# Optimization experiments

Measured on AMD Instinct MI355X. Metric: run time of the kernel, lower is better.

The kernel has to match this reference:

```python
import jax, jax.numpy as jnp
import numpy as np

N_EXPERTS = 64
TOP_K = 8
NORM_TOPK = True
SCALING = 1.0


def setup_inputs() -> dict:
    key = jax.random.key(0)
    logits = jax.random.normal(key, (524288, N_EXPERTS), dtype=jnp.float32)
    return {"logits": logits}


def reference(logits):
    # scoring_func == 'softmax': softmax over expert dim in float32
    routing_weights = jax.nn.softmax(logits.astype(jnp.float32), axis=1)
    # top-k experts per token: values and indices, sorted descending (matches torch.topk)
    topk_weights, topk_ids = jax.lax.top_k(routing_weights, TOP_K)  # [T, K]
    if NORM_TOPK:
        topk_weights = topk_weights / jnp.sum(topk_weights, axis=-1, keepdims=True)
    if SCALING != 1.0:
        topk_weights = topk_weights * SCALING
    # torch.histc(topk_ids, bins=E, min=0, max=E) == bincount over flat ids (float output)
    tokens_per_expert = jnp.zeros((N_EXPERTS,), dtype=jnp.float32).at[topk_ids.ravel()].add(1.0)
    return (logits, routing_weights, topk_weights, topk_ids, tokens_per_expert)
```

## Files before the change

kernel.cpp:

```cpp
#include <hip/hip_runtime.h>
#include <math.h>

#define NEXP 64
#define TOPK 8
#define TTILE 256
#define PITCH 65
#define NPROD 4
#define BLKT 512
#define GRID 256

typedef float v4 __attribute__((ext_vector_type(4)));

#define FAST_BAR() do {                                       \
    __builtin_amdgcn_sched_barrier(0);                        \
    asm volatile("s_waitcnt lgkmcnt(0)" ::: "memory");        \
    __builtin_amdgcn_s_barrier();                             \
    __builtin_amdgcn_sched_barrier(0);                        \
} while (0)

__global__ __launch_bounds__(BLKT) void router_kernel(
    const float* __restrict__ logits,
    float* __restrict__ out_logits,
    float* __restrict__ out_rw,
    float* __restrict__ out_tw,
    float* __restrict__ out_ti,
    float* __restrict__ out_hist,
    int nT)
{
    __shared__ float lds[2][TTILE * PITCH];
    __shared__ float srow[2][TTILE];
    __shared__ float shist[NEXP];

    const int tid  = threadIdx.x;
    const int wid  = tid >> 6;
    const int l    = tid & 63;
    const bool prod = wid < NPROD;
    if (tid < NEXP) shist[tid] = 0.0f;

    const int G = gridDim.x;
    int tb = blockIdx.x;
    v4 regs[16];

    if (prod && tb < nT) {
        const long base = (long)tb * (TTILE * NEXP / 4);
        const v4* g = (const v4*)logits + base;
        #pragma unroll
        for (int k = 0; k < 16; ++k)
            regs[k] = __builtin_nontemporal_load(&g[(wid << 6) + l + (k << 8)]);
        v4* gp = (v4*)out_logits + base;
        #pragma unroll
        for (int k = 0; k < 16; ++k) {
            int i = (wid << 6) + l + (k << 8);
            v4 v = regs[k];
            gp[i] = v;
            int r = i >> 4, c4 = (i & 15) << 2;
            float* b = &lds[0][r * PITCH + c4];
            b[0] = v.x; b[1] = v.y; b[2] = v.z; b[3] = v.w;
        }
    }
    FAST_BAR();

    int it = 0;
    for (; tb < nT; ++it, tb += G) {
        const int cur = it & 1;
        const int nxt = cur ^ 1;
        const int tb_next = tb + G;

        if (prod) {
            if (tb_next < nT) {
                const v4* g = (const v4*)logits + (long)tb_next * (TTILE * NEXP / 4);
                #pragma unroll
                for (int k = 0; k < 16; ++k)
                    regs[k] = __builtin_nontemporal_load(&g[(wid << 6) + l + (k << 8)]);
            }
            if (it > 0) {
                v4* grw = (v4*)out_rw + (long)(tb - G) * (TTILE * NEXP / 4);
                #pragma unroll
                for (int k = 0; k < 16; ++k) {
                    int i = (wid << 6) + l + (k << 8);
                    int r = i >> 4, c4 = (i & 15) << 2;
                    float si = srow[nxt][r];
                    const float* b = &lds[nxt][r * PITCH + c4];
                    v4 o = { b[0] * si, b[1] * si, b[2] * si, b[3] * si };
                    grw[i] = o;
                }
            }
            if (tb_next < nT) {
                v4* gp = (v4*)out_logits + (long)tb_next * (TTILE * NEXP / 4);
                #pragma unroll
                for (int k = 0; k < 16; ++k) {
                    int i = (wid << 6) + l + (k << 8);
                    v4 v = regs[k];
                    gp[i] = v;
                    int r = i >> 4, c4 = (i & 15) << 2;
                    float* b = &lds[nxt][r * PITCH + c4];
                    b[0] = v.x; b[1] = v.y; b[2] = v.z; b[3] = v.w;
                }
            }
        } else {
            const int t = ((wid - NPROD) << 6) + l;
            float* __restrict__ row = &lds[cur][t * PITCH];
            float vals[TOPK], ids[TOPK];
            #pragma unroll
            for (int j = 0; j < TOPK; ++j) { vals[j] = -INFINITY; ids[j] = 0.0f; }
            float ssum = 0.0f;

            #pragma unroll 8
            for (int e = 0; e < NEXP; ++e) {
                float x  = row[e];
                float ev = __expf(x);
                ssum += ev;
                row[e] = ev;
                float fe = (float)e;
                bool c[TOPK];
                #pragma unroll
                for (int j = 0; j < TOPK; ++j) c[j] = x > vals[j];
                #pragma unroll
                for (int j = TOPK - 1; j >= 1; --j) {
                    ids[j]  = c[j] ? (c[j - 1] ? ids[j - 1] : fe) : ids[j];
                    vals[j] = __builtin_amdgcn_fmed3f(x, vals[j - 1], vals[j]);
                }
                ids[0]  = c[0] ? fe : ids[0];
                vals[0] = fmaxf(vals[0], x);
            }
            const float sinv = 1.0f / ssum;
            srow[cur][t] = sinv;

            float ew[TOPK];
            float tsum = 0.0f;
            #pragma unroll
            for (int j = 0; j < TOPK; ++j) { ew[j] = __expf(vals[j]); tsum += ew[j]; }
            const float tinv = 1.0f / tsum;

            const long tok = (long)tb * TTILE + t;
            v4* twp = (v4*)out_tw + tok * 2;
            v4* tip = (v4*)out_ti + tok * 2;
            v4 w0 = { ew[0] * tinv, ew[1] * tinv, ew[2] * tinv, ew[3] * tinv };
            v4 w1 = { ew[4] * tinv, ew[5] * tinv, ew[6] * tinv, ew[7] * tinv };
            v4 i0 = { ids[0], ids[1], ids[2], ids[3] };
            v4 i1 = { ids[4], ids[5], ids[6], ids[7] };
            twp[0] = w0; twp[1] = w1;
            tip[0] = i0; tip[1] = i1;

            #pragma unroll
            for (int j = 0; j < TOPK; ++j)
                atomicAdd(&shist[(int)ids[j]], 1.0f);
        }
        FAST_BAR();
    }

    if (prod && it > 0) {
        const int lastpar = (it - 1) & 1;
        v4* grw = (v4*)out_rw + (long)(tb - G) * (TTILE * NEXP / 4);
        #pragma unroll
        for (int k = 0; k < 16; ++k) {
            int i = (wid << 6) + l + (k << 8);
            int r = i >> 4, c4 = (i & 15) << 2;
            float si = srow[lastpar][r];
            const float* b = &lds[lastpar][r * PITCH + c4];
            v4 o = { b[0] * si, b[1] * si, b[2] * si, b[3] * si };
            grw[i] = o;
        }
    }
    __syncthreads();
    if (tid < NEXP) atomicAdd(&out_hist[tid], shist[tid]);
}

extern "C" void kernel_launch(void* const* d_in, const int* in_sizes, int n_in,
                              void* d_out, int out_size, void* d_ws, size_t ws_size,
                              hipStream_t stream) {
    const float* logits = (const float*)d_in[0];
    const long T = (long)in_sizes[0] / NEXP;

    float* out      = (float*)d_out;
    float* o_logits = out;
    float* o_rw     = out + T * NEXP;
    float* o_tw     = out + 2 * T * NEXP;
    float* o_ti     = o_tw + T * TOPK;
    float* o_hist   = o_ti + T * TOPK;

    (void)hipMemsetAsync(o_hist, 0, NEXP * sizeof(float), stream);

    const int nT   = (int)(T / TTILE);
    const int grid = nT < GRID ? nT : GRID;
    router_kernel<<<grid, BLKT, 0, stream>>>(logits, o_logits, o_rw, o_tw, o_ti,
                                             o_hist, nT);
}
```

Baseline: 88.76 us.

## Move routing-weight writeback from producer waves into consumer waves

```diff
diff --git a/kernel.cpp b/kernel.cpp
--- a/kernel.cpp
+++ b/kernel.cpp
@@ -28,7 +28,6 @@
     int nT)
 {
     __shared__ float lds[2][TTILE * PITCH];
-    __shared__ float srow[2][TTILE];
     __shared__ float shist[NEXP];
 
     const int tid  = threadIdx.x;
@@ -72,20 +71,6 @@
                 #pragma unroll
                 for (int k = 0; k < 16; ++k)
                     regs[k] = __builtin_nontemporal_load(&g[(wid << 6) + l + (k << 8)]);
-            }
-            if (it > 0) {
-                v4* grw = (v4*)out_rw + (long)(tb - G) * (TTILE * NEXP / 4);
-                #pragma unroll
-                for (int k = 0; k < 16; ++k) {
-                    int i = (wid << 6) + l + (k << 8);
-                    int r = i >> 4, c4 = (i & 15) << 2;
-                    float si = srow[nxt][r];
-                    const float* b = &lds[nxt][r * PITCH + c4];
-                    v4 o = { b[0] * si, b[1] * si, b[2] * si, b[3] * si };
-                    grw[i] = o;
-                }
-            }
-            if (tb_next < nT) {
                 v4* gp = (v4*)out_logits + (long)tb_next * (TTILE * NEXP / 4);
                 #pragma unroll
                 for (int k = 0; k < 16; ++k) {
@@ -98,7 +83,8 @@
                 }
             }
         } else {
-            const int t = ((wid - NPROD) << 6) + l;
+            const int cw = wid - NPROD;
+            const int t  = (cw << 6) + l;
             float* __restrict__ row = &lds[cur][t * PITCH];
             float vals[TOPK], ids[TOPK];
             #pragma unroll
@@ -124,7 +110,6 @@
                 vals[0] = fmaxf(vals[0], x);
             }
             const float sinv = 1.0f / ssum;
-            srow[cur][t] = sinv;
 
             float ew[TOPK];
             float tsum = 0.0f;
@@ -145,24 +130,22 @@
             #pragma unroll
             for (int j = 0; j < TOPK; ++j)
                 atomicAdd(&shist[(int)ids[j]], 1.0f);
+
+            v4* grw = (v4*)out_rw + ((long)tb * TTILE + (cw << 6)) * (NEXP / 4);
+            #pragma unroll
+            for (int k = 0; k < 16; ++k) {
+                int il   = l + (k << 6);
+                int rsub = il >> 4;
+                int c4   = (il & 15) << 2;
+                float si = __shfl(sinv, rsub);
+                const float* b = &lds[cur][((cw << 6) + rsub) * PITCH + c4];
+                v4 o = { b[0] * si, b[1] * si, b[2] * si, b[3] * si };
+                grw[il] = o;
+            }
         }
         FAST_BAR();
     }
 
-    if (prod && it > 0) {
-        const int lastpar = (it - 1) & 1;
-        v4* grw = (v4*)out_rw + (long)(tb - G) * (TTILE * NEXP / 4);
-        #pragma unroll
-        for (int k = 0; k < 16; ++k) {
-            int i = (wid << 6) + l + (k << 8);
-            int r = i >> 4, c4 = (i & 15) << 2;
-            float si = srow[lastpar][r];
-            const float* b = &lds[lastpar][r * PITCH + c4];
-            v4 o = { b[0] * si, b[1] * si, b[2] * si, b[3] * si };
-            grw[i] = o;
-        }
-    }
-    __syncthreads();
     if (tid < NEXP) atomicAdd(&out_hist[tid], shist[tid]);
 }
 
```

After: 91.73 us. 1.03x slower.
